# Optimization experiments

Hardware: AMD Instinct MI355X
Metric: run time of the kernel (lower is better)

## Reference

```python
import jax, jax.numpy as jnp
import numpy as np

E = 768      # embed_dim (hidden_size)
H = 12       # num_attention_heads
DH = E // H  # head_dim = 64
B, S = 8, 1024


def setup_inputs() -> dict:
    key = jax.random.key(0)
    ks = jax.random.split(key, 10)
    sc = 1.0 / np.sqrt(E)
    inp = {
        "hidden_state": jax.random.normal(ks[0], (B, S, E), dtype=jnp.float32),
        # per-head Q/K/V projections, stacked over heads: [H, E, DH]
        "Wq": jax.random.normal(ks[1], (H, E, DH), dtype=jnp.float32) * sc,
        "bq": jax.random.normal(ks[2], (H, DH), dtype=jnp.float32) * 0.02,
        "Wk": jax.random.normal(ks[3], (H, E, DH), dtype=jnp.float32) * sc,
        "bk": jax.random.normal(ks[4], (H, DH), dtype=jnp.float32) * 0.02,
        "Wv": jax.random.normal(ks[5], (H, E, DH), dtype=jnp.float32) * sc,
        "bv": jax.random.normal(ks[6], (H, DH), dtype=jnp.float32) * 0.02,
        # output projection: [E, E]
        "Wo": jax.random.normal(ks[7], (E, E), dtype=jnp.float32) * sc,
        "bo": jax.random.normal(ks[8], (E,), dtype=jnp.float32) * 0.02,
    }
    return inp


def reference(hidden_state, Wq, bq, Wk, bk, Wv, bv, Wo, bo):
    # Q/K/V per head: [B,S,E] x [H,E,D] -> [B,H,S,D]
    q = jnp.einsum("bse,hed->bhsd", hidden_state, Wq) + bq[None, :, None, :]
    k = jnp.einsum("bse,hed->bhsd", hidden_state, Wk) + bk[None, :, None, :]
    v = jnp.einsum("bse,hed->bhsd", hidden_state, Wv) + bv[None, :, None, :]
    scale = 1.0 / jnp.sqrt(jnp.asarray(DH, dtype=q.dtype))
    scores = jnp.einsum("bhsd,bhtd->bhst", q, k) * scale   # [B,H,S,S]
    weights = jax.nn.softmax(scores, axis=-1)
    attn = jnp.einsum("bhst,bhtd->bhsd", weights, v)        # [B,H,S,D]
    # concat heads (head order matches ModuleList concat): [B,S,H*D]=[B,S,E]
    x = attn.transpose(0, 2, 1, 3).reshape(hidden_state.shape[0], hidden_state.shape[1], E)
    return x @ Wo + bo
```

## Files before the change

### kernel.cpp

```cpp
#include <hip/hip_runtime.h>

typedef unsigned short u16;
typedef __bf16 bf16;
typedef bf16 bf16x8 __attribute__((ext_vector_type(8)));
typedef float f32x4 __attribute__((ext_vector_type(4)));
typedef u16 u16x4 __attribute__((ext_vector_type(4)));
typedef u16 u16x8 __attribute__((ext_vector_type(8)));

#define MROWS 8192
#define EDIM 768
#define NQKV 2304
#define NHEAD 12
#define DH 64
#define SEQ 1024
#define BATCH 8
#define BH 96
#define BHSD (BH * SEQ * DH)
#define KITERS (EDIM / 32)
#define TBUF (128 * 32)

__device__ __forceinline__ u16 f2bf(float f) {
  union { float f; unsigned u; } v; v.f = f;
  unsigned r = v.u + 0x7fffu + ((v.u >> 16) & 1u);
  return (u16)(r >> 16);
}

#define GLDS16(g, l)                                                          \
  __builtin_amdgcn_global_load_lds(                                           \
      (const __attribute__((address_space(1))) void*)(g),                     \
      (__attribute__((address_space(3))) void*)(l), 16, 0, 0)


__global__ void cvt_x(const float* __restrict__ x, u16* __restrict__ xb, int n) {
  int i = (blockIdx.x * blockDim.x + threadIdx.x) * 4;
  if (i >= n) return;
  float4 v = *(const float4*)(x + i);
  u16x4 o;
  o[0] = f2bf(v.x); o[1] = f2bf(v.y); o[2] = f2bf(v.z); o[3] = f2bf(v.w);
  *(u16x4*)(xb + i) = o;
}

__global__ __launch_bounds__(256) void pack_w(
    const float* __restrict__ Wq, const float* __restrict__ Wk,
    const float* __restrict__ Wv, const float* __restrict__ Wo,
    u16* __restrict__ Wt, u16* __restrict__ Wot) {
  __shared__ float T[64][65];
  int bid = blockIdx.x;
  int tid = threadIdx.x;
  int c = tid & 63, r4 = tid >> 6;
  if (bid < 432) {
    int region = bid / 144, rem = bid - region * 144;
    int h = rem / 12, e0 = (rem - h * 12) * 64;
    const float* W = region == 0 ? Wq : (region == 1 ? Wk : Wv);
    for (int p = 0; p < 16; p++) {
      int er = r4 + p * 4;
      T[er][c] = W[(size_t)(h * EDIM + e0 + er) * DH + c];
    }
    __syncthreads();
    int nbase = region * EDIM + h * 64;
    for (int p = 0; p < 16; p++) {
      int dr = r4 + p * 4;
      Wt[(size_t)(nbase + dr) * EDIM + e0 + c] = f2bf(T[c][dr]);
    }
  } else {
    bid -= 432;
    int n0 = (bid / 12) * 64, e0 = (bid - (bid / 12) * 12) * 64;
    for (int p = 0; p < 16; p++) {
      int er = r4 + p * 4;
      T[er][c] = Wo[(size_t)(e0 + er) * EDIM + n0 + c];
    }
    __syncthreads();
    for (int p = 0; p < 16; p++) {
      int dr = r4 + p * 4;
      Wot[(size_t)(n0 + dr) * EDIM + e0 + c] = f2bf(T[c][dr]);
    }
  }
}

__device__ __forceinline__ void gemm_core(
    const u16* __restrict__ A, const u16* __restrict__ Bt,
    u16* As, u16* Bs,
    int m0, int n0, int tid, f32x4 acc[4][4]) {
  int wv = __builtin_amdgcn_readfirstlane(tid >> 6);
  int lane = tid & 63, quad = lane >> 4, l16 = lane & 15;
  int wm = (wv & 1) * 64, wn = (wv >> 1) * 64;
  int srow = wv * 32 + (lane >> 2);
  int schunk = (lane & 3) ^ ((lane >> 3) & 3);
  const u16* Ag = A + (size_t)(m0 + srow) * EDIM + schunk * 8;
  const u16* Bg = Bt + (size_t)(n0 + srow) * EDIM + schunk * 8;
  int sboff = wv * 32 * 32;
  int fragoff = (quad ^ ((l16 >> 1) & 3)) * 8;

  GLDS16(Ag, As + sboff);
  GLDS16(Ag + 16 * EDIM, As + sboff + 16 * 32);
  GLDS16(Bg, Bs + sboff);
  GLDS16(Bg + 16 * EDIM, Bs + sboff + 16 * 32);

  for (int k = 0; k < KITERS; k++) {
    int cur = (k & 1) * TBUF, nxt = ((k + 1) & 1) * TBUF;
    __syncthreads();
    if (k + 1 < KITERS) {
      int ko = (k + 1) * 32;
      GLDS16(Ag + ko, As + nxt + sboff);
      GLDS16(Ag + ko + 16 * EDIM, As + nxt + sboff + 16 * 32);
      GLDS16(Bg + ko, Bs + nxt + sboff);
      GLDS16(Bg + ko + 16 * EDIM, Bs + nxt + sboff + 16 * 32);
    }
    bf16x8 af[4], bfr[4];
    for (int i = 0; i < 4; i++)
      af[i] = *(const bf16x8*)(As + cur + (wm + i * 16 + l16) * 32 + fragoff);
    for (int j = 0; j < 4; j++)
      bfr[j] = *(const bf16x8*)(Bs + cur + (wn + j * 16 + l16) * 32 + fragoff);
    for (int i = 0; i < 4; i++)
      for (int j = 0; j < 4; j++)
        acc[i][j] = __builtin_amdgcn_mfma_f32_16x16x32_bf16(af[i], bfr[j], acc[i][j], 0, 0, 0);
  }
}

__global__ __launch_bounds__(256, 4) void gemm_qkv(
    const u16* __restrict__ A, const u16* __restrict__ Bt,
    const float* __restrict__ bq, const float* __restrict__ bk, const float* __restrict__ bv,
    u16* __restrict__ qkv) {
  __shared__ u16 As[2 * TBUF];
  __shared__ u16 Bs[2 * TBUF];
  int tid = threadIdx.x;
  int wv = tid >> 6, lane = tid & 63, quad = lane >> 4, l16 = lane & 15;
  int wm = (wv & 1) * 64, wn = (wv >> 1) * 64;
  int m0 = blockIdx.x * 128, n0 = blockIdx.y * 128;
  f32x4 acc[4][4] = {};
  gemm_core(A, Bt, As, Bs, m0, n0, tid, acc);

  const float kQscale = 0.18033688011112042f;
  for (int i = 0; i < 4; i++) {
    int row0 = m0 + wm + i * 16 + quad * 4;
    for (int j = 0; j < 4; j++) {
      int n = n0 + wn + j * 16 + l16;
      int region = n / EDIM;
      int hd = n - region * EDIM;
      int h = hd >> 6, d = hd & 63;
      const float* bp = region == 0 ? bq : (region == 1 ? bk : bv);
      float bias = bp[hd];
      float scale = region == 0 ? kQscale : 1.0f;
      for (int r = 0; r < 4; r++) {
        int rr = row0 + r;
        int bb = rr >> 10, s = rr & 1023;
        float val = (acc[i][j][r] + bias) * scale;
        u16 bv16 = f2bf(val);
        int bhh = bb * NHEAD + h;
        if (region < 2) {
          qkv[(size_t)region * BHSD + ((size_t)bhh * SEQ + s) * DH + d] = bv16;
        } else {
          qkv[(size_t)2 * BHSD + ((size_t)bhh * DH + d) * SEQ + s] = bv16;
        }
      }
    }
  }
}

__global__ __launch_bounds__(256) void attn_kernel(const u16* __restrict__ qkv, u16* __restrict__ attn) {
  int bh = blockIdx.y;
  int b = bh / NHEAD, h = bh - b * NHEAD;
  const u16* Q  = qkv + (size_t)bh * SEQ * DH;
  const u16* K  = qkv + (size_t)(BH + bh) * SEQ * DH;
  const u16* VT = qkv + (size_t)(2 * BH + bh) * SEQ * DH;
  int tid = threadIdx.x, wave = tid >> 6, lane = tid & 63, quad = lane >> 4, l16 = lane & 15;
  int q_base = blockIdx.x * 128 + wave * 32;

  __shared__ u16 Ks[32 * 72];
  __shared__ u16 Vts[64 * 40];
  __shared__ u16 Ps[4][32 * 40];

  bf16x8 qf[2][2];
  for (int qi = 0; qi < 2; qi++)
    for (int c = 0; c < 2; c++)
      qf[qi][c] = *(const bf16x8*)(Q + (size_t)(q_base + qi * 16 + l16) * DH + c * 32 + quad * 8);

  f32x4 o[2][4] = {};
  float l_i[2][4] = {};

  int tr = tid >> 3, tc8 = (tid & 7) * 8;
  int vr = tid >> 2, vc8 = (tid & 3) * 8;

  for (int t0 = 0; t0 < SEQ; t0 += 32) {
    u16x8 kv = *(const u16x8*)(K + (size_t)(t0 + tr) * DH + tc8);
    u16x8 vv = *(const u16x8*)(VT + (size_t)vr * SEQ + t0 + vc8);
    __syncthreads();
    *(u16x8*)(Ks + tr * 72 + tc8) = kv;
    *(u16x8*)(Vts + vr * 40 + vc8) = vv;
    __syncthreads();

    bf16x8 kf[2][2];
    for (int tc = 0; tc < 2; tc++)
      for (int c = 0; c < 2; c++)
        kf[tc][c] = *(const bf16x8*)(Ks + (tc * 16 + l16) * 72 + c * 32 + quad * 8);

    float p[2][2][4];
    for (int qi = 0; qi < 2; qi++)
      for (int tc = 0; tc < 2; tc++) {
        f32x4 z = {};
        z = __builtin_amdgcn_mfma_f32_16x16x32_bf16(qf[qi][0], kf[tc][0], z, 0, 0, 0);
        z = __builtin_amdgcn_mfma_f32_16x16x32_bf16(qf[qi][1], kf[tc][1], z, 0, 0, 0);
        for (int r = 0; r < 4; r++) {
          float e = exp2f(z[r]);
          p[qi][tc][r] = e;
          l_i[qi][r] += e;
        }
      }

    u16* P = Ps[wave];
    for (int qi = 0; qi < 2; qi++)
      for (int tc = 0; tc < 2; tc++)
        for (int r = 0; r < 4; r++)
          P[(qi * 16 + quad * 4 + r) * 40 + tc * 16 + l16] = f2bf(p[qi][tc][r]);
    bf16x8 pf[2];
    for (int qi = 0; qi < 2; qi++)
      pf[qi] = *(const bf16x8*)(P + (qi * 16 + l16) * 40 + quad * 8);

    bf16x8 vf[4];
    for (int n = 0; n < 4; n++)
      vf[n] = *(const bf16x8*)(Vts + (n * 16 + l16) * 40 + quad * 8);

    for (int qi = 0; qi < 2; qi++)
      for (int n = 0; n < 4; n++)
        o[qi][n] = __builtin_amdgcn_mfma_f32_16x16x32_bf16(pf[qi], vf[n], o[qi][n], 0, 0, 0);
  }

  for (int qi = 0; qi < 2; qi++)
    for (int r = 0; r < 4; r++) {
      float s = l_i[qi][r];
      for (int mask = 1; mask <= 8; mask <<= 1)
        s += __shfl_xor(s, mask);
      l_i[qi][r] = s;
    }

  for (int qi = 0; qi < 2; qi++)
    for (int r = 0; r < 4; r++) {
      float inv = 1.0f / l_i[qi][r];
      int qrow = q_base + qi * 16 + quad * 4 + r;
      size_t rowoff = (size_t)(b * SEQ + qrow) * EDIM + h * DH;
      for (int n = 0; n < 4; n++)
        attn[rowoff + n * 16 + l16] = f2bf(o[qi][n][r] * inv);
    }
}

__global__ __launch_bounds__(256, 4) void gemm_out(
    const u16* __restrict__ A, const u16* __restrict__ Bt,
    const float* __restrict__ bo, float* __restrict__ out) {
  __shared__ u16 As[2 * TBUF];
  __shared__ u16 Bs[2 * TBUF];
  int tid = threadIdx.x;
  int wv = tid >> 6, lane = tid & 63, quad = lane >> 4, l16 = lane & 15;
  int wm = (wv & 1) * 64, wn = (wv >> 1) * 64;
  int m0 = blockIdx.x * 128, n0 = blockIdx.y * 128;
  f32x4 acc[4][4] = {};
  gemm_core(A, Bt, As, Bs, m0, n0, tid, acc);

  for (int i = 0; i < 4; i++) {
    int row0 = m0 + wm + i * 16 + quad * 4;
    for (int j = 0; j < 4; j++) {
      int n = n0 + wn + j * 16 + l16;
      float bias = bo[n];
      for (int r = 0; r < 4; r++)
        out[(size_t)(row0 + r) * EDIM + n] = acc[i][j][r] + bias;
    }
  }
}

extern "C" void kernel_launch(void* const* d_in, const int* in_sizes, int n_in,
                              void* d_out, int out_size, void* d_ws, size_t ws_size,
                              hipStream_t stream) {
  const float* x  = (const float*)d_in[0];
  const float* Wq = (const float*)d_in[1];
  const float* bq = (const float*)d_in[2];
  const float* Wk = (const float*)d_in[3];
  const float* bk = (const float*)d_in[4];
  const float* Wv = (const float*)d_in[5];
  const float* bv = (const float*)d_in[6];
  const float* Wo = (const float*)d_in[7];
  const float* bo = (const float*)d_in[8];
  float* out = (float*)d_out;
  char* ws = (char*)d_ws;

  u16* Xb   = (u16*)(ws);
  u16* Wt   = (u16*)(ws + 12582912);
  u16* Wot  = (u16*)(ws + 16121856);
  u16* qkv  = (u16*)(ws + 17301504);
  u16* attn = (u16*)(ws + 55050240);

  cvt_x<<<6144, 256, 0, stream>>>(x, Xb, MROWS * EDIM);
  pack_w<<<576, 256, 0, stream>>>(Wq, Wk, Wv, Wo, Wt, Wot);
  gemm_qkv<<<dim3(64, 18), 256, 0, stream>>>(Xb, Wt, bq, bk, bv, qkv);
  attn_kernel<<<dim3(8, 96), 256, 0, stream>>>(qkv, attn);
  gemm_out<<<dim3(64, 6), 256, 0, stream>>>(attn, Wot, bo, out);
}
```

Baseline: 228.7 us.

## Use single-wave 64x64 GEMM blocks with vmcnt waits instead of barriers

Both projection GEMMs now run as one-wavefront blocks, each computing a 64x64 tile, in place of 256-thread blocks computing 128x128 tiles. The __syncthreads in the K loop is replaced by explicit s_waitcnt vmcnt on the direct global-to-LDS loads, so no workgroup barrier is needed. The grid grows fourfold and the QKV epilogue hoists the region, head and bias-pointer logic per block. This removes barrier stalls and may raise occupancy, but each tile gets half the operand reuse, so global and L2 traffic per FLOP doubles.

```diff
diff --git a/kernel.cpp b/kernel.cpp
--- a/kernel.cpp
+++ b/kernel.cpp
@@ -17,7 +17,7 @@
 #define BH 96
 #define BHSD (BH * SEQ * DH)
 #define KITERS (EDIM / 32)
-#define TBUF (128 * 32)
+#define WBUF (64 * 32)
 
 __device__ __forceinline__ u16 f2bf(float f) {
   union { float f; unsigned u; } v; v.f = f;
@@ -77,70 +77,69 @@
   }
 }
 
-__device__ __forceinline__ void gemm_core(
+__device__ __forceinline__ void gemm_core_w(
     const u16* __restrict__ A, const u16* __restrict__ Bt,
     u16* As, u16* Bs,
-    int m0, int n0, int tid, f32x4 acc[4][4]) {
-  int wv = __builtin_amdgcn_readfirstlane(tid >> 6);
-  int lane = tid & 63, quad = lane >> 4, l16 = lane & 15;
-  int wm = (wv & 1) * 64, wn = (wv >> 1) * 64;
-  int srow = wv * 32 + (lane >> 2);
+    int m0, int n0, int lane, f32x4 acc[4][4]) {
+  int quad = lane >> 4, l16 = lane & 15;
+  int srow = lane >> 2;
   int schunk = (lane & 3) ^ ((lane >> 3) & 3);
   const u16* Ag = A + (size_t)(m0 + srow) * EDIM + schunk * 8;
   const u16* Bg = Bt + (size_t)(n0 + srow) * EDIM + schunk * 8;
-  int sboff = wv * 32 * 32;
   int fragoff = (quad ^ ((l16 >> 1) & 3)) * 8;
 
-  GLDS16(Ag, As + sboff);
-  GLDS16(Ag + 16 * EDIM, As + sboff + 16 * 32);
-  GLDS16(Bg, Bs + sboff);
-  GLDS16(Bg + 16 * EDIM, Bs + sboff + 16 * 32);
-
+  for (int g = 0; g < 4; g++) {
+    GLDS16(Ag + g * 16 * EDIM, As + g * 512);
+    GLDS16(Bg + g * 16 * EDIM, Bs + g * 512);
+  }
   for (int k = 0; k < KITERS; k++) {
-    int cur = (k & 1) * TBUF, nxt = ((k + 1) & 1) * TBUF;
-    __syncthreads();
+    const u16* Asc = As + (k & 1) * WBUF;
+    const u16* Bsc = Bs + (k & 1) * WBUF;
     if (k + 1 < KITERS) {
+      u16* Asn = As + ((k + 1) & 1) * WBUF;
+      u16* Bsn = Bs + ((k + 1) & 1) * WBUF;
       int ko = (k + 1) * 32;
-      GLDS16(Ag + ko, As + nxt + sboff);
-      GLDS16(Ag + ko + 16 * EDIM, As + nxt + sboff + 16 * 32);
-      GLDS16(Bg + ko, Bs + nxt + sboff);
-      GLDS16(Bg + ko + 16 * EDIM, Bs + nxt + sboff + 16 * 32);
+      for (int g = 0; g < 4; g++) {
+        GLDS16(Ag + ko + g * 16 * EDIM, Asn + g * 512);
+        GLDS16(Bg + ko + g * 16 * EDIM, Bsn + g * 512);
+      }
+      __asm__ volatile("s_waitcnt vmcnt(8)" ::: "memory");
+    } else {
+      __asm__ volatile("s_waitcnt vmcnt(0)" ::: "memory");
     }
     bf16x8 af[4], bfr[4];
     for (int i = 0; i < 4; i++)
-      af[i] = *(const bf16x8*)(As + cur + (wm + i * 16 + l16) * 32 + fragoff);
+      af[i] = *(const bf16x8*)(Asc + (i * 16 + l16) * 32 + fragoff);
     for (int j = 0; j < 4; j++)
-      bfr[j] = *(const bf16x8*)(Bs + cur + (wn + j * 16 + l16) * 32 + fragoff);
+      bfr[j] = *(const bf16x8*)(Bsc + (j * 16 + l16) * 32 + fragoff);
     for (int i = 0; i < 4; i++)
       for (int j = 0; j < 4; j++)
         acc[i][j] = __builtin_amdgcn_mfma_f32_16x16x32_bf16(af[i], bfr[j], acc[i][j], 0, 0, 0);
   }
 }
 
-__global__ __launch_bounds__(256, 4) void gemm_qkv(
+__global__ __launch_bounds__(64) void gemm_qkv(
     const u16* __restrict__ A, const u16* __restrict__ Bt,
     const float* __restrict__ bq, const float* __restrict__ bk, const float* __restrict__ bv,
     u16* __restrict__ qkv) {
-  __shared__ u16 As[2 * TBUF];
-  __shared__ u16 Bs[2 * TBUF];
-  int tid = threadIdx.x;
-  int wv = tid >> 6, lane = tid & 63, quad = lane >> 4, l16 = lane & 15;
-  int wm = (wv & 1) * 64, wn = (wv >> 1) * 64;
-  int m0 = blockIdx.x * 128, n0 = blockIdx.y * 128;
+  __shared__ u16 As[2 * WBUF];
+  __shared__ u16 Bs[2 * WBUF];
+  int lane = threadIdx.x, quad = lane >> 4, l16 = lane & 15;
+  int m0 = blockIdx.x * 64, n0 = blockIdx.y * 64;
   f32x4 acc[4][4] = {};
-  gemm_core(A, Bt, As, Bs, m0, n0, tid, acc);
+  gemm_core_w(A, Bt, As, Bs, m0, n0, lane, acc);
 
   const float kQscale = 0.18033688011112042f;
+  int region = n0 / EDIM;
+  int hd0 = n0 - region * EDIM;
+  int h = hd0 >> 6;
+  const float* bp = region == 0 ? bq : (region == 1 ? bk : bv);
+  float scale = region == 0 ? kQscale : 1.0f;
   for (int i = 0; i < 4; i++) {
-    int row0 = m0 + wm + i * 16 + quad * 4;
+    int row0 = m0 + i * 16 + quad * 4;
     for (int j = 0; j < 4; j++) {
-      int n = n0 + wn + j * 16 + l16;
-      int region = n / EDIM;
-      int hd = n - region * EDIM;
-      int h = hd >> 6, d = hd & 63;
-      const float* bp = region == 0 ? bq : (region == 1 ? bk : bv);
-      float bias = bp[hd];
-      float scale = region == 0 ? kQscale : 1.0f;
+      int d = j * 16 + l16;
+      float bias = bp[hd0 + d];
       for (int r = 0; r < 4; r++) {
         int rr = row0 + r;
         int bb = rr >> 10, s = rr & 1023;
@@ -243,22 +242,20 @@
     }
 }
 
-__global__ __launch_bounds__(256, 4) void gemm_out(
+__global__ __launch_bounds__(64) void gemm_out(
     const u16* __restrict__ A, const u16* __restrict__ Bt,
     const float* __restrict__ bo, float* __restrict__ out) {
-  __shared__ u16 As[2 * TBUF];
-  __shared__ u16 Bs[2 * TBUF];
-  int tid = threadIdx.x;
-  int wv = tid >> 6, lane = tid & 63, quad = lane >> 4, l16 = lane & 15;
-  int wm = (wv & 1) * 64, wn = (wv >> 1) * 64;
-  int m0 = blockIdx.x * 128, n0 = blockIdx.y * 128;
+  __shared__ u16 As[2 * WBUF];
+  __shared__ u16 Bs[2 * WBUF];
+  int lane = threadIdx.x, quad = lane >> 4, l16 = lane & 15;
+  int m0 = blockIdx.x * 64, n0 = blockIdx.y * 64;
   f32x4 acc[4][4] = {};
-  gemm_core(A, Bt, As, Bs, m0, n0, tid, acc);
+  gemm_core_w(A, Bt, As, Bs, m0, n0, lane, acc);
 
   for (int i = 0; i < 4; i++) {
-    int row0 = m0 + wm + i * 16 + quad * 4;
+    int row0 = m0 + i * 16 + quad * 4;
     for (int j = 0; j < 4; j++) {
-      int n = n0 + wn + j * 16 + l16;
+      int n = n0 + j * 16 + l16;
       float bias = bo[n];
       for (int r = 0; r < 4; r++)
         out[(size_t)(row0 + r) * EDIM + n] = acc[i][j][r] + bias;
@@ -289,7 +286,7 @@
 
   cvt_x<<<6144, 256, 0, stream>>>(x, Xb, MROWS * EDIM);
   pack_w<<<576, 256, 0, stream>>>(Wq, Wk, Wv, Wo, Wt, Wot);
-  gemm_qkv<<<dim3(64, 18), 256, 0, stream>>>(Xb, Wt, bq, bk, bv, qkv);
+  gemm_qkv<<<dim3(128, 36), 64, 0, stream>>>(Xb, Wt, bq, bk, bv, qkv);
   attn_kernel<<<dim3(8, 96), 256, 0, stream>>>(qkv, attn);
-  gemm_out<<<dim3(64, 6), 256, 0, stream>>>(attn, Wot, bo, out);
-}
+  gemm_out<<<dim3(128, 12), 64, 0, stream>>>(attn, Wot, bo, out);
+}
```

Measured after the change: 246.9 us. 7.9% more time.

## Load GEMM fragments directly from global into registers, dropping LDS staging

Applied to the files above, without the earlier changes.

Both projection GEMMs now read MFMA operand fragments straight from global memory into double-buffered registers instead of staging tiles through shared memory with async global-to-LDS copies. This removes the per-iteration barrier and the shared-memory traffic. Each wave now fetches its own fragments, so tiles shared across the block's waves are read from global/L2 several times, with 16-byte accesses that are only partially coalesced. Launch bounds drop the occupancy hint from 4 to 3 blocks to leave room for the extra registers.

```diff
diff --git a/kernel.cpp b/kernel.cpp
--- a/kernel.cpp
+++ b/kernel.cpp
@@ -17,18 +17,12 @@
 #define BH 96
 #define BHSD (BH * SEQ * DH)
 #define KITERS (EDIM / 32)
-#define TBUF (128 * 32)
 
 __device__ __forceinline__ u16 f2bf(float f) {
   union { float f; unsigned u; } v; v.f = f;
   unsigned r = v.u + 0x7fffu + ((v.u >> 16) & 1u);
   return (u16)(r >> 16);
 }
-
-#define GLDS16(g, l)                                                          \
-  __builtin_amdgcn_global_load_lds(                                           \
-      (const __attribute__((address_space(1))) void*)(g),                     \
-      (__attribute__((address_space(3))) void*)(l), 16, 0, 0)
 
 
 __global__ void cvt_x(const float* __restrict__ x, u16* __restrict__ xb, int n) {
@@ -77,58 +71,45 @@
   }
 }
 
-__device__ __forceinline__ void gemm_core(
+__device__ __forceinline__ void gemm_core_reg(
     const u16* __restrict__ A, const u16* __restrict__ Bt,
-    u16* As, u16* Bs,
     int m0, int n0, int tid, f32x4 acc[4][4]) {
   int wv = __builtin_amdgcn_readfirstlane(tid >> 6);
   int lane = tid & 63, quad = lane >> 4, l16 = lane & 15;
   int wm = (wv & 1) * 64, wn = (wv >> 1) * 64;
-  int srow = wv * 32 + (lane >> 2);
-  int schunk = (lane & 3) ^ ((lane >> 3) & 3);
-  const u16* Ag = A + (size_t)(m0 + srow) * EDIM + schunk * 8;
-  const u16* Bg = Bt + (size_t)(n0 + srow) * EDIM + schunk * 8;
-  int sboff = wv * 32 * 32;
-  int fragoff = (quad ^ ((l16 >> 1) & 3)) * 8;
-
-  GLDS16(Ag, As + sboff);
-  GLDS16(Ag + 16 * EDIM, As + sboff + 16 * 32);
-  GLDS16(Bg, Bs + sboff);
-  GLDS16(Bg + 16 * EDIM, Bs + sboff + 16 * 32);
-
+  const u16* Ag = A + (size_t)(m0 + wm + l16) * EDIM + quad * 8;
+  const u16* Bg = Bt + (size_t)(n0 + wn + l16) * EDIM + quad * 8;
+
+  bf16x8 af[2][4], bfr[2][4];
+  for (int i = 0; i < 4; i++) {
+    af[0][i]  = *(const bf16x8*)(Ag + i * 16 * EDIM);
+    bfr[0][i] = *(const bf16x8*)(Bg + i * 16 * EDIM);
+  }
   for (int k = 0; k < KITERS; k++) {
-    int cur = (k & 1) * TBUF, nxt = ((k + 1) & 1) * TBUF;
-    __syncthreads();
+    int cur = k & 1, nxt = cur ^ 1;
     if (k + 1 < KITERS) {
       int ko = (k + 1) * 32;
-      GLDS16(Ag + ko, As + nxt + sboff);
-      GLDS16(Ag + ko + 16 * EDIM, As + nxt + sboff + 16 * 32);
-      GLDS16(Bg + ko, Bs + nxt + sboff);
-      GLDS16(Bg + ko + 16 * EDIM, Bs + nxt + sboff + 16 * 32);
-    }
-    bf16x8 af[4], bfr[4];
-    for (int i = 0; i < 4; i++)
-      af[i] = *(const bf16x8*)(As + cur + (wm + i * 16 + l16) * 32 + fragoff);
-    for (int j = 0; j < 4; j++)
-      bfr[j] = *(const bf16x8*)(Bs + cur + (wn + j * 16 + l16) * 32 + fragoff);
+      for (int i = 0; i < 4; i++) {
+        af[nxt][i]  = *(const bf16x8*)(Ag + ko + i * 16 * EDIM);
+        bfr[nxt][i] = *(const bf16x8*)(Bg + ko + i * 16 * EDIM);
+      }
+    }
     for (int i = 0; i < 4; i++)
       for (int j = 0; j < 4; j++)
-        acc[i][j] = __builtin_amdgcn_mfma_f32_16x16x32_bf16(af[i], bfr[j], acc[i][j], 0, 0, 0);
-  }
-}
-
-__global__ __launch_bounds__(256, 4) void gemm_qkv(
+        acc[i][j] = __builtin_amdgcn_mfma_f32_16x16x32_bf16(af[cur][i], bfr[cur][j], acc[i][j], 0, 0, 0);
+  }
+}
+
+__global__ __launch_bounds__(256, 3) void gemm_qkv(
     const u16* __restrict__ A, const u16* __restrict__ Bt,
     const float* __restrict__ bq, const float* __restrict__ bk, const float* __restrict__ bv,
     u16* __restrict__ qkv) {
-  __shared__ u16 As[2 * TBUF];
-  __shared__ u16 Bs[2 * TBUF];
   int tid = threadIdx.x;
   int wv = tid >> 6, lane = tid & 63, quad = lane >> 4, l16 = lane & 15;
   int wm = (wv & 1) * 64, wn = (wv >> 1) * 64;
   int m0 = blockIdx.x * 128, n0 = blockIdx.y * 128;
   f32x4 acc[4][4] = {};
-  gemm_core(A, Bt, As, Bs, m0, n0, tid, acc);
+  gemm_core_reg(A, Bt, m0, n0, tid, acc);
 
   const float kQscale = 0.18033688011112042f;
   for (int i = 0; i < 4; i++) {
@@ -243,17 +224,15 @@
     }
 }
 
-__global__ __launch_bounds__(256, 4) void gemm_out(
+__global__ __launch_bounds__(256, 3) void gemm_out(
     const u16* __restrict__ A, const u16* __restrict__ Bt,
     const float* __restrict__ bo, float* __restrict__ out) {
-  __shared__ u16 As[2 * TBUF];
-  __shared__ u16 Bs[2 * TBUF];
   int tid = threadIdx.x;
   int wv = tid >> 6, lane = tid & 63, quad = lane >> 4, l16 = lane & 15;
   int wm = (wv & 1) * 64, wn = (wv >> 1) * 64;
   int m0 = blockIdx.x * 128, n0 = blockIdx.y * 128;
   f32x4 acc[4][4] = {};
-  gemm_core(A, Bt, As, Bs, m0, n0, tid, acc);
+  gemm_core_reg(A, Bt, m0, n0, tid, acc);
 
   for (int i = 0; i < 4; i++) {
     int row0 = m0 + wm + i * 16 + quad * 4;
```

Result: slower. 329.4 us (+44.0%).
